# Performance work log

Hardware: AMD Instinct MI355X
Metric: run time of the kernel (lower is better)

Reference implementation:

```python
import jax, jax.numpy as jnp
import numpy as np

D_IN = 1024
D_OUT = 1024
N_HEADS = 16
HEAD_DIM = D_IN // N_HEADS      # 64
HEAD_DIM_V = D_OUT // N_HEADS   # 64


def setup_inputs() -> dict:
    key = jax.random.key(0)
    ks = jax.random.split(key, 7)
    s = 0.02
    x = jax.random.normal(ks[0], (4, 2048, D_IN), dtype=jnp.float32)
    Wq = jax.random.normal(ks[1], (D_IN, D_IN), dtype=jnp.float32) * s
    bq = jnp.zeros((D_IN,), dtype=jnp.float32)
    Wk = jax.random.normal(ks[2], (D_IN, D_IN), dtype=jnp.float32) * s
    bk = jnp.zeros((D_IN,), dtype=jnp.float32)
    Wv = jax.random.normal(ks[3], (D_IN, D_OUT), dtype=jnp.float32) * s
    bv = jnp.zeros((D_OUT,), dtype=jnp.float32)
    return {"x": x, "Wq": Wq, "bq": bq, "Wk": Wk, "bk": bk, "Wv": Wv, "bv": bv}


def reference(x, Wq, bq, Wk, bk, Wv, bv):
    B, S, _ = x.shape
    scale = jnp.sqrt(jnp.asarray(HEAD_DIM, dtype=jnp.float32))
    # projections -> [B, S, H, Dh] -> [B, H, S, Dh]
    q = (x @ Wq + bq).reshape(B, S, N_HEADS, HEAD_DIM).transpose(0, 2, 1, 3)
    k = (x @ Wk + bk).reshape(B, S, N_HEADS, HEAD_DIM).transpose(0, 2, 1, 3)
    v = (x @ Wv + bv).reshape(B, S, N_HEADS, HEAD_DIM_V).transpose(0, 2, 1, 3)
    # [B, H, S, S] attention scores (naive full materialization, as in source)
    scores = jnp.einsum("bhsd,bhtd->bhst", q, k) / scale
    weights = jax.nn.softmax(scores, axis=-1)
    out = jnp.einsum("bhst,bhtd->bhsd", weights, v)
    # [B, H, S, Dv] -> [B, S, H*Dv]  (out_projection NOT applied in source forward)
    return out.transpose(0, 2, 1, 3).reshape(B, S, N_HEADS * HEAD_DIM_V)
```

## Files before the change

### kernel.cpp

```cpp
#include <hip/hip_runtime.h>

#define B_  4
#define S_  2048
#define D_  1024
#define H_  16
#define DH_ 64
#define M_  (B_ * S_)

typedef __attribute__((ext_vector_type(8))) short short8;
typedef __attribute__((ext_vector_type(4))) float floatx4;

__device__ __forceinline__ float bf2f(unsigned short u) {
    union { unsigned int i; float f; } v; v.i = ((unsigned int)u) << 16; return v.f;
}
__device__ __forceinline__ unsigned short f2bf(float f) {
    union { float f; unsigned int i; } v; v.f = f;
    unsigned int r = v.i + 0x7fffu + ((v.i >> 16) & 1u);
    return (unsigned short)(r >> 16);
}
__device__ __forceinline__ unsigned int pk_trunc(float a, float b) {
#if __has_builtin(__builtin_amdgcn_perm)
    return __builtin_amdgcn_perm(__float_as_uint(b), __float_as_uint(a), 0x07060302u);
#else
    return (__float_as_uint(a) >> 16) | (__float_as_uint(b) & 0xffff0000u);
#endif
}

#if __has_builtin(__builtin_amdgcn_exp2f)
#define EXP2(x) __builtin_amdgcn_exp2f(x)
#else
#define EXP2(x) __expf(0.6931471805599453f * (x))
#endif

typedef const __attribute__((address_space(1))) unsigned int* gas_ptr;
typedef __attribute__((address_space(3))) unsigned int* las_ptr;
__device__ __forceinline__ void async_cp16(const void* g, void* l) {
    __builtin_amdgcn_global_load_lds((gas_ptr)g, (las_ptr)l, 16, 0, 0);
}

#define VMC3 asm volatile("s_waitcnt vmcnt(3)" ::: "memory")
#define VMC0 asm volatile("s_waitcnt vmcnt(0)" ::: "memory")

__global__ __launch_bounds__(256) void cast_fused_kernel(
    const float* __restrict__ x, unsigned short* __restrict__ Ax,
    const float* __restrict__ W0, const float* __restrict__ W1,
    const float* __restrict__ W2,
    unsigned short* __restrict__ T0, unsigned short* __restrict__ T1,
    unsigned short* __restrict__ T2)
{
    const int bid = blockIdx.x;
    const int t = threadIdx.x;
    if (bid < 8192) {
        int i4 = bid * 256 + t;
        float4 v = reinterpret_cast<const float4*>(x)[i4];
        ushort4 o;
        o.x = f2bf(v.x); o.y = f2bf(v.y); o.z = f2bf(v.z); o.w = f2bf(v.w);
        reinterpret_cast<ushort4*>(Ax)[i4] = o;
        return;
    }
    const int idx = bid - 8192;
    const int z   = idx >> 8;
    const int rem = idx & 255;
    const float* W = z == 0 ? W0 : (z == 1 ? W1 : W2);
    unsigned short* Wt = z == 0 ? T0 : (z == 1 ? T1 : T2);

    __shared__ unsigned short T[64][72];
    const int k0 = (rem & 15) * 64, n0 = (rem >> 4) * 64;

    #pragma unroll
    for (int p = 0; p < 4; ++p) {
        int kr = p * 16 + (t >> 4);
        int nc = (t & 15) * 4;
        float4 v = *reinterpret_cast<const float4*>(W + (size_t)(k0 + kr) * D_ + n0 + nc);
        T[nc + 0][kr] = f2bf(v.x);
        T[nc + 1][kr] = f2bf(v.y);
        T[nc + 2][kr] = f2bf(v.z);
        T[nc + 3][kr] = f2bf(v.w);
    }
    __syncthreads();

    const int nl = t >> 2, kc = (t & 3) * 16;
    size_t base = (size_t)(n0 + nl) * D_ + k0 + kc;
    *reinterpret_cast<short8*>(Wt + base)     = *reinterpret_cast<const short8*>(&T[nl][kc]);
    *reinterpret_cast<short8*>(Wt + base + 8) = *reinterpret_cast<const short8*>(&T[nl][kc + 8]);
}

__global__ __launch_bounds__(512) void gemm_qkv_mfma(
    const unsigned short* __restrict__ Ax,
    const unsigned short* __restrict__ Wt,
    const float* __restrict__ bq, const float* __restrict__ bk,
    const float* __restrict__ bv,
    unsigned short* __restrict__ Q,
    unsigned short* __restrict__ Vtg)
{
    __shared__ unsigned short lds[49152];

    const int tid  = threadIdx.x;
    const int lane = tid & 63;
    const int w    = tid >> 6;
    const int wm   = w >> 2;
    const int wn   = w & 3;
    const int l15  = lane & 15, quad = lane >> 4;

    const int pl   = tid >> 3;
    const int sl   = tid & 7;
    const int xx   = sl ^ (pl & 7);
    const int sro  = pl * 2 + (xx >> 2);
    const int sc   = (xx & 3) * 8;
    const int ldst = tid * 8;
    const int fb = (l15 >> 1) * 64 + ((((l15 & 1) << 2) | quad) ^ (l15 >> 1)) * 8;

    const int id  = blockIdx.x;
    const int g   = (id & 7) * 96 + (id >> 3);
    const int nb  = g >> 6;
    const int mb  = g & 63;
    const int m0  = mb * 128;
    const int n0g = nb * 256;
    const int mat = nb >> 2;
    const int n0m = (nb & 3) * 256;
    const float* bias = mat == 0 ? bq : (mat == 1 ? bk : bv);

    #define ASTG(kcol, reg) \
        async_cp16(Ax + (size_t)(m0 + sro) * 1024 + (kcol) + sc, lds + (reg) + ldst)
    #define BSTG(kcol, reg) do { \
        async_cp16(Wt + (size_t)(n0g + sro) * 1024 + (kcol) + sc,       lds + (reg) + ldst); \
        async_cp16(Wt + (size_t)(n0g + 128 + sro) * 1024 + (kcol) + sc, lds + (reg) + 4096 + ldst); \
    } while (0)

    floatx4 acc[4][4] = {};

    ASTG(0, 0);      BSTG(0, 8192);
    ASTG(32, 4096);  BSTG(32, 16384);
    ASTG(64, 24576); BSTG(64, 32768);
    VMC3;
    __builtin_amdgcn_s_barrier();

    #define PH(bufS, ksub, STAGE_STMT, WAIT_STMT) do { \
        short8 af[4], bfr[4]; \
        _Pragma("unroll") \
        for (int i = 0; i < 4; ++i) \
            af[i] = *reinterpret_cast<const short8*>(lds + (bufS) + (ksub) * 4096 + wm * 2048 + i * 512 + fb); \
        _Pragma("unroll") \
        for (int j = 0; j < 4; ++j) \
            bfr[j] = *reinterpret_cast<const short8*>(lds + (bufS) + 8192 + (ksub) * 8192 + wn * 2048 + j * 512 + fb); \
        STAGE_STMT; \
        __builtin_amdgcn_s_barrier(); \
        asm volatile("s_waitcnt lgkmcnt(0)" ::: "memory"); \
        __builtin_amdgcn_sched_barrier(0); \
        __builtin_amdgcn_s_setprio(1); \
        _Pragma("unroll") \
        for (int i = 0; i < 4; ++i) \
            _Pragma("unroll") \
            for (int j = 0; j < 4; ++j) \
                acc[i][j] = __builtin_amdgcn_mfma_f32_16x16x32_bf16(af[i], bfr[j], acc[i][j], 0, 0, 0); \
        __builtin_amdgcn_s_setprio(0); \
        WAIT_STMT; \
        __builtin_amdgcn_s_barrier(); \
    } while (0)

    #pragma unroll 1
    for (int it = 0; it < 8; ++it) {
        const bool nl = (it < 7);
        const int  kA = (2 * it + 1) * 64;
        const int  kB = kA + 64;
        const int  kC = kA + 128;
        PH(0,     0, { ASTG(kA + 32, 28672); BSTG(kA + 32, 40960); }, );
        PH(0,     1, if (nl) { ASTG(kB, 0); BSTG(kB, 8192); }, { if (nl) VMC3; else VMC0; });
        PH(24576, 0, if (nl) { ASTG(kB + 32, 4096); BSTG(kB + 32, 16384); }, );
        PH(24576, 1, if (nl) { ASTG(kC, 24576); BSTG(kC, 32768); }, { if (nl) VMC3; });
    }

    float bb[4];
    #pragma unroll
    for (int j = 0; j < 4; ++j) bb[j] = bias[n0m + wn * 64 + j * 16 + l15];

    if (mat == 2) {
        const int bI    = m0 >> 11;
        #pragma unroll
        for (int i = 0; i < 4; ++i) {
            int srow = (m0 & 2047) + wm * 64 + i * 16 + quad * 4;
            #pragma unroll
            for (int j = 0; j < 4; ++j) {
                int col = n0m + wn * 64 + j * 16 + l15;
                ushort4 o;
                o.x = f2bf(acc[i][j][0] + bb[j]);
                o.y = f2bf(acc[i][j][1] + bb[j]);
                o.z = f2bf(acc[i][j][2] + bb[j]);
                o.w = f2bf(acc[i][j][3] + bb[j]);
                *reinterpret_cast<ushort4*>(Vtg + (size_t)(bI * 1024 + col) * S_ + srow) = o;
            }
        }
    } else {
        unsigned short* C = Q + (size_t)mat * M_ * D_;
        const float scq = (mat == 0) ? 0.18033688011112042f : 1.0f;
        #pragma unroll
        for (int i = 0; i < 4; ++i)
            #pragma unroll
            for (int r = 0; r < 4; ++r) {
                int row = m0 + wm * 64 + i * 16 + quad * 4 + r;
                #pragma unroll
                for (int j = 0; j < 4; ++j)
                    C[(size_t)row * D_ + n0m + wn * 64 + j * 16 + l15] = f2bf((acc[i][j][r] + bb[j]) * scq);
            }
    }
}

#define KT_   64
#define PITCH 72

__global__ __launch_bounds__(256, 4) void attn_mfma(
    const unsigned short* __restrict__ Qg,
    const unsigned short* __restrict__ Kg,
    const unsigned short* __restrict__ Vtg,
    float* __restrict__ out)
{
    __shared__ unsigned short Ks[KT_ * PITCH];
    __shared__ unsigned short Vt[DH_ * PITCH];

    const int tid  = threadIdx.x;
    const int wq   = tid >> 6;
    const int lane = tid & 63;
    const int l15  = lane & 15;
    const int quad = lane >> 4;

    const int id  = blockIdx.x;
    const int bh  = (id & 7) * 8 + ((id >> 3) & 7);
    const int qt  = id >> 6;
    const int b   = bh >> 4;
    const int colbase = (bh & 15) * DH_;
    const int rowQ0 = b * S_ + qt * 128;

    short8 qf[2][2];
    #pragma unroll
    for (int g = 0; g < 2; ++g) {
        int qrow = rowQ0 + wq * 32 + g * 16 + l15;
        qf[g][0] = *reinterpret_cast<const short8*>(Qg + (size_t)qrow * D_ + colbase + quad * 8);
        qf[g][1] = *reinterpret_cast<const short8*>(Qg + (size_t)qrow * D_ + colbase + 32 + quad * 8);
    }

    short8 vones;
    #pragma unroll
    for (int i = 0; i < 8; ++i) vones[i] = (short)0x3F80;

    floatx4 Oacc[2][4] = {};
    floatx4 Lacc[2] = {};

    const int srow = tid >> 3;
    const int sc8  = (tid & 7) * 8;
    const int vc  = sc8 >> 4;
    const int vqk = (sc8 >> 2) & 3;
    const int vk0 = ((vc & 1) << 2) + ((vc >> 1) << 5) + (vqk << 3);

    const unsigned short* Kbase = Kg + (size_t)(b * S_) * D_ + colbase;
    const unsigned short* Vbase = Vtg + (size_t)(bh * 64) * S_;

    short8 kpre[2], vpre[2];
    #pragma unroll
    for (int p = 0; p < 2; ++p) {
        kpre[p] = *reinterpret_cast<const short8*>(Kbase + (size_t)(p * 32 + srow) * D_ + sc8);
        vpre[p] = *reinterpret_cast<const short8*>(Vbase + (size_t)(p * 32 + srow) * S_ + sc8);
    }

    for (int kt = 0; kt < S_ / KT_; ++kt) {
        __syncthreads();
        #pragma unroll
        for (int p = 0; p < 2; ++p) {
            *reinterpret_cast<short8*>(&Ks[(p * 32 + srow) * PITCH + sc8]) = kpre[p];
            uint4 u = __builtin_bit_cast(uint4, vpre[p]);
            uint2 lo, hi;
            lo.x = u.x; lo.y = u.y; hi.x = u.z; hi.y = u.w;
            *reinterpret_cast<uint2*>(&Vt[(p * 32 + srow) * PITCH + vk0])     = lo;
            *reinterpret_cast<uint2*>(&Vt[(p * 32 + srow) * PITCH + vk0 + 8]) = hi;
        }
        if (kt + 1 < S_ / KT_) {
            int off = (kt + 1) * KT_;
            #pragma unroll
            for (int p = 0; p < 2; ++p) {
                kpre[p] = *reinterpret_cast<const short8*>(Kbase + (size_t)(off + p * 32 + srow) * D_ + sc8);
                vpre[p] = *reinterpret_cast<const short8*>(Vbase + (size_t)(p * 32 + srow) * S_ + off + sc8);
            }
        }
        __syncthreads();

        #pragma unroll
        for (int half = 0; half < 2; ++half) {
            floatx4 s_[2][2];
            #pragma unroll
            for (int ci = 0; ci < 2; ++ci) {
                int c = half * 2 + ci;
                short8 kf0 = *reinterpret_cast<const short8*>(&Ks[(c * 16 + l15) * PITCH + quad * 8]);
                short8 kf1 = *reinterpret_cast<const short8*>(&Ks[(c * 16 + l15) * PITCH + 32 + quad * 8]);
                #pragma unroll
                for (int g = 0; g < 2; ++g) {
                    floatx4 a = {0.f, 0.f, 0.f, 0.f};
                    a = __builtin_amdgcn_mfma_f32_16x16x32_bf16(kf0, qf[g][0], a, 0, 0, 0);
                    a = __builtin_amdgcn_mfma_f32_16x16x32_bf16(kf1, qf[g][1], a, 0, 0, 0);
                    s_[g][ci] = a;
                }
            }
            short8 pa[2];
            #pragma unroll
            for (int g = 0; g < 2; ++g) {
                float p00 = EXP2(s_[g][0][0]), p01 = EXP2(s_[g][0][1]);
                float p02 = EXP2(s_[g][0][2]), p03 = EXP2(s_[g][0][3]);
                float p10 = EXP2(s_[g][1][0]), p11 = EXP2(s_[g][1][1]);
                float p12 = EXP2(s_[g][1][2]), p13 = EXP2(s_[g][1][3]);
                uint4 pu;
                pu.x = pk_trunc(p00, p01);
                pu.y = pk_trunc(p02, p03);
                pu.z = pk_trunc(p10, p11);
                pu.w = pk_trunc(p12, p13);
                pa[g] = __builtin_bit_cast(short8, pu);
            }
            #pragma unroll
            for (int g = 0; g < 2; ++g)
                Lacc[g] = __builtin_amdgcn_mfma_f32_16x16x32_bf16(pa[g], vones, Lacc[g], 0, 0, 0);
            #pragma unroll
            for (int d = 0; d < 4; ++d) {
                short8 vf = *reinterpret_cast<const short8*>(
                    &Vt[(d * 16 + l15) * PITCH + half * 32 + quad * 8]);
                #pragma unroll
                for (int g = 0; g < 2; ++g)
                    Oacc[g][d] = __builtin_amdgcn_mfma_f32_16x16x32_bf16(pa[g], vf, Oacc[g][d], 0, 0, 0);
            }
        }
    }

    #pragma unroll
    for (int g = 0; g < 2; ++g) {
        int orow = rowQ0 + wq * 32 + g * 16 + quad * 4;
        #pragma unroll
        for (int r = 0; r < 4; ++r) {
            float inv = 1.f / Lacc[g][r];
            #pragma unroll
            for (int d = 0; d < 4; ++d)
                out[(size_t)(orow + r) * D_ + colbase + d * 16 + l15] = Oacc[g][d][r] * inv;
        }
    }
}

extern "C" void kernel_launch(void* const* d_in, const int* in_sizes, int n_in,
                              void* d_out, int out_size, void* d_ws, size_t ws_size,
                              hipStream_t stream) {
    const float* x  = (const float*)d_in[0];
    const float* Wq = (const float*)d_in[1];
    const float* bq = (const float*)d_in[2];
    const float* Wk = (const float*)d_in[3];
    const float* bk = (const float*)d_in[4];
    const float* Wv = (const float*)d_in[5];
    const float* bv = (const float*)d_in[6];
    float* out = (float*)d_out;

    unsigned short* Q   = (unsigned short*)d_ws;
    unsigned short* K   = Q + (size_t)M_ * D_;
    unsigned short* Vtg = K + (size_t)M_ * D_;
    unsigned short* Ax  = Vtg + (size_t)M_ * D_;
    unsigned short* Wtq = Ax + (size_t)M_ * D_;
    unsigned short* Wtk = Wtq + (size_t)D_ * D_;
    unsigned short* Wtv = Wtk + (size_t)D_ * D_;

    cast_fused_kernel<<<8192 + 768, 256, 0, stream>>>(x, Ax, Wq, Wk, Wv, Wtq, Wtk, Wtv);

    gemm_qkv_mfma<<<768, 512, 0, stream>>>(Ax, Wtq, bq, bk, bv, Q, Vtg);

    attn_mfma<<<1024, 256, 0, stream>>>(Q, K, Vtg, out);
}
```

Baseline: 228.8 us.

## Load K fragments directly from global into registers, bypassing shared memory

Drops the shared-memory K tile. Each wave now loads its MFMA K fragments straight from global memory into registers and prefetches the next tile's fragments right after the QK MFMAs for each half. This removes the LDS write/read traffic for K and shrinks LDS use. In exchange, every wave loads the same K data redundantly from global or L2 with less coalesced 16-byte row accesses, and register pressure rises.

```diff
diff --git a/kernel.cpp b/kernel.cpp
--- a/kernel.cpp
+++ b/kernel.cpp
@@ -10,9 +10,6 @@
 typedef __attribute__((ext_vector_type(8))) short short8;
 typedef __attribute__((ext_vector_type(4))) float floatx4;
 
-__device__ __forceinline__ float bf2f(unsigned short u) {
-    union { unsigned int i; float f; } v; v.i = ((unsigned int)u) << 16; return v.f;
-}
 __device__ __forceinline__ unsigned short f2bf(float f) {
     union { float f; unsigned int i; } v; v.f = f;
     unsigned int r = v.i + 0x7fffu + ((v.i >> 16) & 1u);
@@ -206,6 +203,7 @@
 }
 
 #define KT_   64
+#define NT_   (S_ / KT_)
 #define PITCH 72
 
 __global__ __launch_bounds__(256, 4) void attn_mfma(
@@ -214,7 +212,6 @@
     const unsigned short* __restrict__ Vtg,
     float* __restrict__ out)
 {
-    __shared__ unsigned short Ks[KT_ * PITCH];
     __shared__ unsigned short Vt[DH_ * PITCH];
 
     const int tid  = threadIdx.x;
@@ -254,31 +251,34 @@
     const unsigned short* Kbase = Kg + (size_t)(b * S_) * D_ + colbase;
     const unsigned short* Vbase = Vtg + (size_t)(bh * 64) * S_;
 
-    short8 kpre[2], vpre[2];
-    #pragma unroll
-    for (int p = 0; p < 2; ++p) {
-        kpre[p] = *reinterpret_cast<const short8*>(Kbase + (size_t)(p * 32 + srow) * D_ + sc8);
+    short8 kf[4][2];
+    #pragma unroll
+    for (int c = 0; c < 4; ++c) {
+        const unsigned short* kr = Kbase + (size_t)(c * 16 + l15) * D_;
+        kf[c][0] = *reinterpret_cast<const short8*>(kr + quad * 8);
+        kf[c][1] = *reinterpret_cast<const short8*>(kr + 32 + quad * 8);
+    }
+
+    short8 vpre[2];
+    #pragma unroll
+    for (int p = 0; p < 2; ++p)
         vpre[p] = *reinterpret_cast<const short8*>(Vbase + (size_t)(p * 32 + srow) * S_ + sc8);
-    }
-
-    for (int kt = 0; kt < S_ / KT_; ++kt) {
+
+    for (int kt = 0; kt < NT_; ++kt) {
         __syncthreads();
         #pragma unroll
         for (int p = 0; p < 2; ++p) {
-            *reinterpret_cast<short8*>(&Ks[(p * 32 + srow) * PITCH + sc8]) = kpre[p];
             uint4 u = __builtin_bit_cast(uint4, vpre[p]);
             uint2 lo, hi;
             lo.x = u.x; lo.y = u.y; hi.x = u.z; hi.y = u.w;
             *reinterpret_cast<uint2*>(&Vt[(p * 32 + srow) * PITCH + vk0])     = lo;
             *reinterpret_cast<uint2*>(&Vt[(p * 32 + srow) * PITCH + vk0 + 8]) = hi;
         }
-        if (kt + 1 < S_ / KT_) {
+        if (kt + 1 < NT_) {
             int off = (kt + 1) * KT_;
             #pragma unroll
-            for (int p = 0; p < 2; ++p) {
-                kpre[p] = *reinterpret_cast<const short8*>(Kbase + (size_t)(off + p * 32 + srow) * D_ + sc8);
+            for (int p = 0; p < 2; ++p)
                 vpre[p] = *reinterpret_cast<const short8*>(Vbase + (size_t)(p * 32 + srow) * S_ + off + sc8);
-            }
         }
         __syncthreads();
 
@@ -288,14 +288,22 @@
             #pragma unroll
             for (int ci = 0; ci < 2; ++ci) {
                 int c = half * 2 + ci;
-                short8 kf0 = *reinterpret_cast<const short8*>(&Ks[(c * 16 + l15) * PITCH + quad * 8]);
-                short8 kf1 = *reinterpret_cast<const short8*>(&Ks[(c * 16 + l15) * PITCH + 32 + quad * 8]);
                 #pragma unroll
                 for (int g = 0; g < 2; ++g) {
                     floatx4 a = {0.f, 0.f, 0.f, 0.f};
-                    a = __builtin_amdgcn_mfma_f32_16x16x32_bf16(kf0, qf[g][0], a, 0, 0, 0);
-                    a = __builtin_amdgcn_mfma_f32_16x16x32_bf16(kf1, qf[g][1], a, 0, 0, 0);
+                    a = __builtin_amdgcn_mfma_f32_16x16x32_bf16(kf[c][0], qf[g][0], a, 0, 0, 0);
+                    a = __builtin_amdgcn_mfma_f32_16x16x32_bf16(kf[c][1], qf[g][1], a, 0, 0, 0);
                     s_[g][ci] = a;
+                }
+            }
+            if (kt + 1 < NT_) {
+                int off = (kt + 1) * KT_;
+                #pragma unroll
+                for (int ci = 0; ci < 2; ++ci) {
+                    int c = half * 2 + ci;
+                    const unsigned short* kr = Kbase + (size_t)(off + c * 16 + l15) * D_;
+                    kf[c][0] = *reinterpret_cast<const short8*>(kr + quad * 8);
+                    kf[c][1] = *reinterpret_cast<const short8*>(kr + 32 + quad * 8);
                 }
             }
             short8 pa[2];
```

Result: slower. 291.3 us (+27.3%).
